# Optimization experiments

Hardware: AMD Instinct MI355X
Metric: run time of the kernel (lower is better)

## Reference

```python
import jax, jax.numpy as jnp
import numpy as np

B, H, W, C_IN, C_HID = 32, 64, 64, 384, 128

def setup_inputs() -> dict:
    key = jax.random.key(0)
    k0, k1, k2 = jax.random.split(key, 3)
    dino_features = jax.random.normal(k0, (B, H, W, C_IN), dtype=jnp.float32)
    # Xavier-uniform(gain=0.5) bounds for conv weights, HWIO layout
    fan1 = C_IN * 9 + C_HID * 9
    lim1 = 0.5 * np.sqrt(6.0 / fan1)
    W1 = jax.random.uniform(k1, (3, 3, C_IN, C_HID), minval=-lim1, maxval=lim1, dtype=jnp.float32)
    b1 = jnp.zeros((C_HID,), dtype=jnp.float32)
    fan2 = C_HID + 1
    lim2 = 0.5 * np.sqrt(6.0 / fan2)
    W2 = jax.random.uniform(k2, (1, 1, C_HID, 1), minval=-lim2, maxval=lim2, dtype=jnp.float32)
    b2 = jnp.zeros((1,), dtype=jnp.float32)
    return {"dino_features": dino_features, "W1": W1, "b1": b1, "W2": W2, "b2": b2}

def _conv(x, w, pad):
    # x: NHWC, w: HWIO -> NHWC
    return jax.lax.conv_general_dilated(
        x, w, window_strides=(1, 1), padding=pad,
        dimension_numbers=("NHWC", "HWIO", "NHWC"))

def reference(dino_features, W1, b1, W2, b2):
    # conv3x3 (pad 1) -> ReLU -> conv1x1 -> sigmoid; output (B,H,W,1)
    h = jax.nn.relu(_conv(dino_features, W1, ((1, 1), (1, 1))) + b1)
    logits = _conv(h, W2, ((0, 0), (0, 0))) + b2
    return jax.nn.sigmoid(logits)
```

## Files before the change

kernel.cpp:

```cpp
#include <hip/hip_runtime.h>
#include <hip/hip_bf16.h>
#include <math.h>


typedef __attribute__((ext_vector_type(8))) unsigned short ushort8;
typedef __attribute__((ext_vector_type(8))) __bf16 bf16x8;
typedef __attribute__((ext_vector_type(4))) float floatx4;

#define HPX 324
#define BUFE 10368

static __device__ __forceinline__ unsigned short f2bf_rne(float f) {
  union { float f; unsigned int u; } x; x.f = f;
  unsigned int u = x.u;
  return (unsigned short)((u + 0x7fffu + ((u >> 16) & 1u)) >> 16);
}

static __device__ __forceinline__ ushort8 pack8(const float* v) {
  ushort8 r;
#pragma unroll
  for (int i = 0; i < 4; ++i) {
    __hip_bfloat162 p = __float22bfloat162_rn(make_float2(v[2 * i], v[2 * i + 1]));
    union { __hip_bfloat162 b; unsigned int u; } c;
    c.b = p;
    r[2 * i] = (unsigned short)(c.u & 0xffffu);
    r[2 * i + 1] = (unsigned short)(c.u >> 16);
  }
  return r;
}

__global__ void prep_w1_kernel(const float* __restrict__ W1,
                               unsigned short* __restrict__ W1b) {
  __shared__ unsigned short tile[32 * 128];
  const int kk = blockIdx.x;
  const int o = kk / 12;
  const int chunk = kk - o * 12;
  const float* src = W1 + (o * 384 + chunk * 32) * 128;
  const int t = threadIdx.x;
#pragma unroll
  for (int i = 0; i < 16; ++i) {
    int idx = t + i * 256;
    int c = idx >> 7;
    int n = idx & 127;
    tile[n * 32 + c] = f2bf_rne(src[idx]);
  }
  __syncthreads();
  unsigned short* dst = W1b + kk * 4096;
#pragma unroll
  for (int i = 0; i < 16; ++i) {
    int idx = t + i * 256;
    dst[idx] = tile[idx];
  }
}

__global__ __launch_bounds__(256, 2) void conv_fused_kernel(
    const float* __restrict__ x, const unsigned short* __restrict__ W1b,
    const float* __restrict__ b1, const float* __restrict__ W2,
    const float* __restrict__ b2, float* __restrict__ out) {
  __shared__ alignas(16) unsigned short Ah[2 * BUFE];
  __shared__ float hsum[256 * 4];

  const int t = threadIdx.x;
  const int w = t >> 6;
  const int lane = t & 63;
  const int g = lane >> 4;
  const int lr = lane & 15;

  const int img = blockIdx.x >> 4;
  const int tileId = blockIdx.x & 15;
  const int ty0 = (tileId >> 2) << 4;
  const int tx0 = (tileId & 3) << 4;

  int smask = 0;
  int soff[6];
#pragma unroll
  for (int j = 0; j < 6; ++j) {
    int item = t + (j << 8);
    int px = item >> 2, sub = item & 3;
    int hy = (px * 57) >> 10;
    int hx = px - hy * 18;
    int iy = ty0 + hy - 1, ix = tx0 + hx - 1;
    int v = (item < 1296) && ((unsigned)iy < 64u) && ((unsigned)ix < 64u);
    smask |= (v << j);
    int iyc = v ? iy : 0, ixc = v ? ix : 0;
    soff[j] = ((((img << 6) + iyc) << 6) + ixc) * 384 + sub * 8;
  }
  const int tsw = t ^ ((t >> 2) & 3);

  const int boff = ((w * 32 + lr) << 5) + (g << 3);
  int lo[4];
#pragma unroll
  for (int q = 0; q < 4; ++q)
    lo[q] = (lr << 5) + ((g ^ ((q + lr) & 3)) << 3);

  floatx4 acc[16][2] = {};

  const float b1v0 = b1[w * 32 + lr];
  const float b1v1 = b1[w * 32 + 16 + lr];
  const float w2v0 = W2[w * 32 + lr];
  const float w2v1 = W2[w * 32 + 16 + lr];

  float sr[3][8];

#pragma unroll
  for (int grp = 0; grp < 2; ++grp) {
#pragma unroll
    for (int j = 0; j < 3; ++j) {
      const int jj = grp * 3 + j;
      if ((smask >> jj) & 1) {
        *(float4*)&sr[j][0] = *(const float4*)(x + soff[jj]);
        *(float4*)&sr[j][4] = *(const float4*)(x + soff[jj] + 4);
      } else {
#pragma unroll
        for (int e = 0; e < 8; ++e) sr[j][e] = 0.0f;
      }
    }
#pragma unroll
    for (int j = 0; j < 3; ++j) {
      const int jj = grp * 3 + j;
      if (jj < 5 || t < 16)
        *(ushort8*)&Ah[(tsw + (jj << 8)) << 3] = pack8(sr[j]);
    }
  }
  __syncthreads();

  for (int c = 0; c < 12; ++c) {
    const int rb = (c & 1) * BUFE;
    const int wb = BUFE - rb;
    const int choff = (c + 1) << 5;
    const bool pf = (c < 11);

#pragma unroll
    for (int ox = 0; ox < 3; ++ox) {
      bf16x8 bf[3][2];
#pragma unroll
      for (int oy = 0; oy < 3; ++oy) {
        const unsigned short* bp =
            W1b + (((oy * 3 + ox) * 12 + c) << 12) + boff;
        bf[oy][0] = *(const bf16x8*)bp;
        bf[oy][1] = *(const bf16x8*)(bp + 512);
      }

      if (ox == 0) {
        if (pf) {
#pragma unroll
          for (int j = 0; j < 3; ++j) {
            if ((smask >> j) & 1) {
              *(float4*)&sr[j][0] = *(const float4*)(x + soff[j] + choff);
              *(float4*)&sr[j][4] = *(const float4*)(x + soff[j] + choff + 4);
            } else {
#pragma unroll
              for (int e = 0; e < 8; ++e) sr[j][e] = 0.0f;
            }
          }
        }
      } else if (ox == 1) {
        if (pf) {
#pragma unroll
          for (int j = 0; j < 3; ++j)
            *(ushort8*)&Ah[wb + ((tsw + (j << 8)) << 3)] = pack8(sr[j]);
#pragma unroll
          for (int j = 0; j < 3; ++j) {
            const int jj = 3 + j;
            if ((smask >> jj) & 1) {
              *(float4*)&sr[j][0] = *(const float4*)(x + soff[jj] + choff);
              *(float4*)&sr[j][4] = *(const float4*)(x + soff[jj] + choff + 4);
            } else {
#pragma unroll
              for (int e = 0; e < 8; ++e) sr[j][e] = 0.0f;
            }
          }
        }
      } else {
        if (pf) {
#pragma unroll
          for (int j = 0; j < 3; ++j) {
            const int jj = 3 + j;
            if (jj < 5 || t < 16)
              *(ushort8*)&Ah[wb + ((tsw + (jj << 8)) << 3)] = pack8(sr[j]);
          }
        }
      }

      __builtin_amdgcn_s_setprio(1);
#pragma unroll
      for (int h = 0; h < 18; ++h) {
        const int P0 = h * 18 + ox;
        const bf16x8 af =
            *(const bf16x8*)&Ah[rb + (P0 << 5) + lo[P0 & 3]];
#pragma unroll
        for (int oy = 0; oy < 3; ++oy) {
          const int mi = h - oy;
          if (mi >= 0 && mi < 16) {
            acc[mi][0] = __builtin_amdgcn_mfma_f32_16x16x32_bf16(
                af, bf[oy][0], acc[mi][0], 0, 0, 0);
            acc[mi][1] = __builtin_amdgcn_mfma_f32_16x16x32_bf16(
                af, bf[oy][1], acc[mi][1], 0, 0, 0);
          }
        }
      }
      __builtin_amdgcn_s_setprio(0);
    }
    __syncthreads();
  }

#pragma unroll
  for (int mi = 0; mi < 16; ++mi) {
#pragma unroll
    for (int r = 0; r < 4; ++r) {
      float h0 = fmaxf(acc[mi][0][r] + b1v0, 0.0f);
      float h1 = fmaxf(acc[mi][1][r] + b1v1, 0.0f);
      float v = h0 * w2v0 + h1 * w2v1;
      v += __shfl_xor(v, 1);
      v += __shfl_xor(v, 2);
      v += __shfl_xor(v, 4);
      v += __shfl_xor(v, 8);
      if (lr == 0) {
        int m = mi * 16 + g * 4 + r;
        hsum[m * 4 + w] = v;
      }
    }
  }
  __syncthreads();
  {
    float s = hsum[t * 4 + 0] + hsum[t * 4 + 1] + hsum[t * 4 + 2] +
              hsum[t * 4 + 3] + b2[0];
    float sig = 1.0f / (1.0f + expf(-s));
    int prow = t >> 4, pcol = t & 15;
    out[((((img << 6) + ty0 + prow) << 6) + tx0 + pcol)] = sig;
  }
}

extern "C" void kernel_launch(void* const* d_in, const int* in_sizes, int n_in,
                              void* d_out, int out_size, void* d_ws, size_t ws_size,
                              hipStream_t stream) {
  const float* x  = (const float*)d_in[0];
  const float* W1 = (const float*)d_in[1];
  const float* b1 = (const float*)d_in[2];
  const float* W2 = (const float*)d_in[3];
  const float* b2 = (const float*)d_in[4];
  float* out = (float*)d_out;
  unsigned short* W1b = (unsigned short*)d_ws;

  prep_w1_kernel<<<108, 256, 0, stream>>>(W1, W1b);
  conv_fused_kernel<<<512, 256, 0, stream>>>(x, W1b, b1, W2, b2, out);
}
```

Measured before the change: 322.6 us.

## Split output channels across eight waves with 512-thread blocks and unswizzled LDS

```diff
diff --git a/kernel.cpp b/kernel.cpp
--- a/kernel.cpp
+++ b/kernel.cpp
@@ -53,12 +53,12 @@
   }
 }
 
-__global__ __launch_bounds__(256, 2) void conv_fused_kernel(
+__global__ __launch_bounds__(512, 4) void conv_fused_kernel(
     const float* __restrict__ x, const unsigned short* __restrict__ W1b,
     const float* __restrict__ b1, const float* __restrict__ W2,
     const float* __restrict__ b2, float* __restrict__ out) {
   __shared__ alignas(16) unsigned short Ah[2 * BUFE];
-  __shared__ float hsum[256 * 4];
+  __shared__ float hsum[256 * 8];
 
   const int t = threadIdx.x;
   const int w = t >> 6;
@@ -72,10 +72,10 @@
   const int tx0 = (tileId & 3) << 4;
 
   int smask = 0;
-  int soff[6];
-#pragma unroll
-  for (int j = 0; j < 6; ++j) {
-    int item = t + (j << 8);
+  int soff[3];
+#pragma unroll
+  for (int j = 0; j < 3; ++j) {
+    int item = t + (j << 9);
     int px = item >> 2, sub = item & 3;
     int hy = (px * 57) >> 10;
     int hx = px - hy * 18;
@@ -85,28 +85,29 @@
     int iyc = v ? iy : 0, ixc = v ? ix : 0;
     soff[j] = ((((img << 6) + iyc) << 6) + ixc) * 384 + sub * 8;
   }
-  const int tsw = t ^ ((t >> 2) & 3);
-
-  const int boff = ((w * 32 + lr) << 5) + (g << 3);
-  int lo[4];
-#pragma unroll
-  for (int q = 0; q < 4; ++q)
-    lo[q] = (lr << 5) + ((g ^ ((q + lr) & 3)) << 3);
-
-  floatx4 acc[16][2] = {};
-
-  const float b1v0 = b1[w * 32 + lr];
-  const float b1v1 = b1[w * 32 + 16 + lr];
-  const float w2v0 = W2[w * 32 + lr];
-  const float w2v1 = W2[w * 32 + 16 + lr];
-
-  float sr[3][8];
-
-#pragma unroll
-  for (int grp = 0; grp < 2; ++grp) {
-#pragma unroll
-    for (int j = 0; j < 3; ++j) {
-      const int jj = grp * 3 + j;
+
+  const int boff = ((w * 16 + lr) << 5) + (g << 3);
+  const int aoffl = (lr << 5) + (g << 3);
+
+  floatx4 acc[16] = {};
+
+  const float b1v = b1[w * 16 + lr];
+  const float w2v = W2[w * 16 + lr];
+
+  float sg1[8];
+  float sr[2][8];
+
+  {
+    if (smask & 1) {
+      *(float4*)&sg1[0] = *(const float4*)(x + soff[0]);
+      *(float4*)&sg1[4] = *(const float4*)(x + soff[0] + 4);
+    } else {
+#pragma unroll
+      for (int e = 0; e < 8; ++e) sg1[e] = 0.0f;
+    }
+#pragma unroll
+    for (int j = 0; j < 2; ++j) {
+      const int jj = 1 + j;
       if ((smask >> jj) & 1) {
         *(float4*)&sr[j][0] = *(const float4*)(x + soff[jj]);
         *(float4*)&sr[j][4] = *(const float4*)(x + soff[jj] + 4);
@@ -115,12 +116,9 @@
         for (int e = 0; e < 8; ++e) sr[j][e] = 0.0f;
       }
     }
-#pragma unroll
-    for (int j = 0; j < 3; ++j) {
-      const int jj = grp * 3 + j;
-      if (jj < 5 || t < 16)
-        *(ushort8*)&Ah[(tsw + (jj << 8)) << 3] = pack8(sr[j]);
-    }
+    *(ushort8*)&Ah[t << 3] = pack8(sg1);
+    *(ushort8*)&Ah[(t + 512) << 3] = pack8(sr[0]);
+    if (t < 272) *(ushort8*)&Ah[(t + 1024) << 3] = pack8(sr[1]);
   }
   __syncthreads();
 
@@ -132,36 +130,30 @@
 
 #pragma unroll
     for (int ox = 0; ox < 3; ++ox) {
-      bf16x8 bf[3][2];
+      bf16x8 bf[3];
 #pragma unroll
       for (int oy = 0; oy < 3; ++oy) {
         const unsigned short* bp =
             W1b + (((oy * 3 + ox) * 12 + c) << 12) + boff;
-        bf[oy][0] = *(const bf16x8*)bp;
-        bf[oy][1] = *(const bf16x8*)(bp + 512);
+        bf[oy] = *(const bf16x8*)bp;
       }
 
       if (ox == 0) {
         if (pf) {
-#pragma unroll
-          for (int j = 0; j < 3; ++j) {
-            if ((smask >> j) & 1) {
-              *(float4*)&sr[j][0] = *(const float4*)(x + soff[j] + choff);
-              *(float4*)&sr[j][4] = *(const float4*)(x + soff[j] + choff + 4);
-            } else {
-#pragma unroll
-              for (int e = 0; e < 8; ++e) sr[j][e] = 0.0f;
-            }
+          if (smask & 1) {
+            *(float4*)&sg1[0] = *(const float4*)(x + soff[0] + choff);
+            *(float4*)&sg1[4] = *(const float4*)(x + soff[0] + choff + 4);
+          } else {
+#pragma unroll
+            for (int e = 0; e < 8; ++e) sg1[e] = 0.0f;
           }
         }
       } else if (ox == 1) {
         if (pf) {
-#pragma unroll
-          for (int j = 0; j < 3; ++j)
-            *(ushort8*)&Ah[wb + ((tsw + (j << 8)) << 3)] = pack8(sr[j]);
-#pragma unroll
-          for (int j = 0; j < 3; ++j) {
-            const int jj = 3 + j;
+          *(ushort8*)&Ah[wb + (t << 3)] = pack8(sg1);
+#pragma unroll
+          for (int j = 0; j < 2; ++j) {
+            const int jj = 1 + j;
             if ((smask >> jj) & 1) {
               *(float4*)&sr[j][0] = *(const float4*)(x + soff[jj] + choff);
               *(float4*)&sr[j][4] = *(const float4*)(x + soff[jj] + choff + 4);
@@ -173,29 +165,22 @@
         }
       } else {
         if (pf) {
-#pragma unroll
-          for (int j = 0; j < 3; ++j) {
-            const int jj = 3 + j;
-            if (jj < 5 || t < 16)
-              *(ushort8*)&Ah[wb + ((tsw + (jj << 8)) << 3)] = pack8(sr[j]);
-          }
+          *(ushort8*)&Ah[wb + ((t + 512) << 3)] = pack8(sr[0]);
+          if (t < 272) *(ushort8*)&Ah[wb + ((t + 1024) << 3)] = pack8(sr[1]);
         }
       }
 
       __builtin_amdgcn_s_setprio(1);
 #pragma unroll
       for (int h = 0; h < 18; ++h) {
-        const int P0 = h * 18 + ox;
         const bf16x8 af =
-            *(const bf16x8*)&Ah[rb + (P0 << 5) + lo[P0 & 3]];
+            *(const bf16x8*)&Ah[rb + ((h * 18 + ox) << 5) + aoffl];
 #pragma unroll
         for (int oy = 0; oy < 3; ++oy) {
           const int mi = h - oy;
           if (mi >= 0 && mi < 16) {
-            acc[mi][0] = __builtin_amdgcn_mfma_f32_16x16x32_bf16(
-                af, bf[oy][0], acc[mi][0], 0, 0, 0);
-            acc[mi][1] = __builtin_amdgcn_mfma_f32_16x16x32_bf16(
-                af, bf[oy][1], acc[mi][1], 0, 0, 0);
+            acc[mi] = __builtin_amdgcn_mfma_f32_16x16x32_bf16(
+                af, bf[oy], acc[mi], 0, 0, 0);
           }
         }
       }
@@ -208,23 +193,23 @@
   for (int mi = 0; mi < 16; ++mi) {
 #pragma unroll
     for (int r = 0; r < 4; ++r) {
-      float h0 = fmaxf(acc[mi][0][r] + b1v0, 0.0f);
-      float h1 = fmaxf(acc[mi][1][r] + b1v1, 0.0f);
-      float v = h0 * w2v0 + h1 * w2v1;
+      float h0 = fmaxf(acc[mi][r] + b1v, 0.0f);
+      float v = h0 * w2v;
       v += __shfl_xor(v, 1);
       v += __shfl_xor(v, 2);
       v += __shfl_xor(v, 4);
       v += __shfl_xor(v, 8);
       if (lr == 0) {
         int m = mi * 16 + g * 4 + r;
-        hsum[m * 4 + w] = v;
+        hsum[m * 8 + w] = v;
       }
     }
   }
   __syncthreads();
-  {
-    float s = hsum[t * 4 + 0] + hsum[t * 4 + 1] + hsum[t * 4 + 2] +
-              hsum[t * 4 + 3] + b2[0];
+  if (t < 256) {
+    float4 p0 = *(const float4*)&hsum[t * 8];
+    float4 p1 = *(const float4*)&hsum[t * 8 + 4];
+    float s = p0.x + p0.y + p0.z + p0.w + p1.x + p1.y + p1.z + p1.w + b2[0];
     float sig = 1.0f / (1.0f + expf(-s));
     int prow = t >> 4, pcol = t & 15;
     out[((((img << 6) + ty0 + prow) << 6) + tx0 + pcol)] = sig;
@@ -243,5 +228,5 @@
   unsigned short* W1b = (unsigned short*)d_ws;
 
   prep_w1_kernel<<<108, 256, 0, stream>>>(W1, W1b);
-  conv_fused_kernel<<<512, 256, 0, stream>>>(x, W1b, b1, W2, b2, out);
-}
+  conv_fused_kernel<<<512, 512, 0, stream>>>(x, W1b, b1, W2, b2, out);
+}
```

After: 320.4 us. No clear change (-0.7%).
